# Kernel tuning notes

Hardware: AMD Instinct MI355X
Metric: run time of the kernel (lower is better)

## Reference

```python
import jax, jax.numpy as jnp
import numpy as np

N = 4096
FIN = 512
HID = 256
NCLS = 2
NE = 131072

def _glorot(key, fan_in, fan_out):
    r = np.sqrt(6.0 / (fan_in + fan_out))
    return jax.random.uniform(key, (fan_in, fan_out), jnp.float32, -r, r)

def setup_inputs() -> dict:
    key = jax.random.key(0)
    ks = jax.random.split(key, 16)
    X = jax.random.normal(ks[0], (N, FIN), jnp.float32)
    adj_rows = jax.random.randint(ks[1], (NE,), 0, N, jnp.int32)
    adj_cols = jax.random.randint(ks[2], (NE,), 0, N, jnp.int32)
    adj_vals = jax.random.uniform(ks[3], (NE,), jnp.float32)
    W_shared = _glorot(ks[4], FIN, HID)
    W_iv = _glorot(ks[5], HID, HID)
    W_c = _glorot(ks[6], HID, HID)
    W_r = _glorot(ks[7], HID, HID)
    Wg_iv = _glorot(ks[8], HID, HID)
    Wg_c = _glorot(ks[9], HID, HID)
    Wg_r = _glorot(ks[10], HID, HID)
    lin_W = _glorot(ks[11], 2 * HID, NCLS)
    lin_b = jnp.zeros((NCLS,), jnp.float32)
    return {"X": X, "adj_rows": adj_rows, "adj_cols": adj_cols, "adj_vals": adj_vals,
            "W_shared": W_shared, "W_iv": W_iv, "W_c": W_c, "W_r": W_r,
            "Wg_iv": Wg_iv, "Wg_c": Wg_c, "Wg_r": Wg_r, "lin_W": lin_W, "lin_b": lin_b}

def _spmm(rows, cols, vals, m):
    # sparse.mm(adj, m): out[i] = sum_{e: rows[e]==i} vals[e] * m[cols[e]]
    return jax.ops.segment_sum(vals[:, None] * m[cols], rows, num_segments=N)

def _gcn(x, rows, cols, vals, W):
    # dropout is identity in eval mode
    return jax.nn.relu(_spmm(rows, cols, vals, x @ W))

def _graphite(x, r1, r2, W):
    h = x @ W
    return jax.nn.relu(r1 @ (r1.T @ h) + r2 @ (r2.T @ h))

def reference(X, adj_rows, adj_cols, adj_vals, W_shared, W_iv, W_c, W_r, Wg_iv, Wg_c, Wg_r, lin_W, lin_b):
    h = _gcn(X, adj_rows, adj_cols, adj_vals, W_shared)
    z_iv0 = _gcn(h, adj_rows, adj_cols, adj_vals, W_iv)
    z_c0 = _gcn(h, adj_rows, adj_cols, adj_vals, W_c)
    z_r0 = _gcn(h, adj_rows, adj_cols, adj_vals, W_r)
    z_iv_rec0 = z_iv0 @ z_iv0.T
    z_c_rec0 = z_c0 @ z_c0.T
    z_r_rec0 = z_r0 @ z_r0.T
    A_dense = jnp.zeros((N, N), jnp.float32).at[adj_rows, adj_cols].add(adj_vals)
    z_iv = _graphite(z_iv0, A_dense, jax.nn.sigmoid(z_iv_rec0), Wg_iv)
    z_c = _graphite(z_c0, A_dense, jax.nn.sigmoid(z_c_rec0), Wg_c)
    z_r = _graphite(z_r0, A_dense, jax.nn.sigmoid(z_r_rec0), Wg_r)
    z_iv_rec = z_iv @ z_iv.T
    z_c_rec = z_c @ z_c.T
    z_r_rec = z_r @ z_r.T
    concat = jnp.concatenate([z_iv, z_c], axis=1)
    pred_T = jax.nn.log_softmax(concat @ lin_W + lin_b, axis=1)
    mi_total_loss = jnp.array(0.0, jnp.float32)
    return (z_iv, z_iv_rec, z_c, z_c_rec, z_r, z_r_rec, mi_total_loss, pred_T)
```

## Files before the change

### kernel.cpp

```cpp
#include <hip/hip_runtime.h>

#define Nn   4096
#define FINd 512
#define HIDd 256
#define NEd  131072

typedef unsigned short u16;
typedef __bf16 bf16x8 __attribute__((ext_vector_type(8)));
typedef float floatx4 __attribute__((ext_vector_type(4)));

__device__ __forceinline__ float bf2f(u16 u) {
  union { unsigned int i; float f; } v; v.i = ((unsigned int)u) << 16; return v.f;
}
__device__ __forceinline__ u16 f2bf(float f) {
  union { unsigned int i; float f; } v; v.f = f;
  unsigned int x = v.i;
  return (u16)((x + 0x7FFFu + ((x >> 16) & 1u)) >> 16);
}

#define GLDS(gp, lp) __builtin_amdgcn_global_load_lds( \
    (__attribute__((address_space(1))) unsigned int*)(void*)(gp), \
    (__attribute__((address_space(3))) unsigned int*)(lp), 16, 0, 0)

__global__ __launch_bounds__(256) void izero_k(int* __restrict__ p, int n) {
  int i = blockIdx.x * 256 + threadIdx.x;
  if (i < n) p[i] = 0;
}

__global__ __launch_bounds__(256) void hist2_k(const int* __restrict__ rows,
                                               const int* __restrict__ cols,
                                               int* __restrict__ rcnt,
                                               int* __restrict__ ccnt) {
  int i = blockIdx.x * 256 + threadIdx.x;
  if (i >= NEd) return;
  atomicAdd(&rcnt[rows[i]], 1);
  atomicAdd(&ccnt[cols[i]], 1);
}

__global__ __launch_bounds__(1024) void scan2_k(const unsigned int* __restrict__ X,
                                                int* __restrict__ cnt,
                                                int* __restrict__ rp, int* __restrict__ cp,
                                                int* __restrict__ flag) {
  __shared__ int part[1024];
  __shared__ int dcnt;
  const int t = threadIdx.x;
  if (t == 0) dcnt = 0;
  __syncthreads();
  int local = 0;
  for (int i = t; i < 4096; i += 1024) {
    unsigned e = (X[i] >> 7) & 0xFFu;
    if (e >= 100u && e <= 140u) local++;
  }
  if (local) atomicAdd(&dcnt, local);
  int base = t * 8, s = 0, loc[8];
#pragma unroll
  for (int j = 0; j < 8; ++j) { loc[j] = s; s += cnt[base + j]; }
  part[t] = s;
  __syncthreads();
  if (t == 0) *flag = (dcnt > 2458) ? 1 : 0;
  for (int off = 1; off < 1024; off <<= 1) {
    int v = (t >= off) ? part[t - off] : 0;
    __syncthreads();
    part[t] += v;
    __syncthreads();
  }
  int excl = (t == 0) ? 0 : part[t - 1];
  int rtot = part[511];
  if (t < 512) {
#pragma unroll
    for (int j = 0; j < 8; ++j) rp[base + j] = excl + loc[j];
    if (t == 511) rp[4096] = rtot;
  } else {
    int cb = base - 4096;
    int ex2 = excl - rtot;
#pragma unroll
    for (int j = 0; j < 8; ++j) cp[cb + j] = ex2 + loc[j];
    if (t == 1023) cp[4096] = part[1023] - rtot;
  }
  for (int i = t; i < 8192; i += 1024) cnt[i] = 0;
}

__global__ __launch_bounds__(256) void scatter2_k(const int* __restrict__ rows,
                                                  const int* __restrict__ cols,
                                                  const void* __restrict__ vals,
                                                  const int* __restrict__ rp,
                                                  const int* __restrict__ cp,
                                                  int* __restrict__ rfill, int* __restrict__ cfill,
                                                  int* __restrict__ recol, float* __restrict__ reval,
                                                  int* __restrict__ cecol, float* __restrict__ ceval,
                                                  const int* __restrict__ flag) {
  int i = blockIdx.x * 256 + threadIdx.x;
  if (i >= NEd) return;
  float v = (*flag) ? bf2f(((const u16*)vals)[i]) : ((const float*)vals)[i];
  int r = rows[i], c = cols[i];
  int p1 = rp[r] + atomicAdd(&rfill[r], 1);
  recol[p1] = c; reval[p1] = v;
  int p2 = cp[c] + atomicAdd(&cfill[c], 1);
  cecol[p2] = r; ceval[p2] = v;
}

__global__ __launch_bounds__(256) void setup_cvt_k(const void* __restrict__ X,
                                                   const void* __restrict__ Wsh,
                                                   const void* __restrict__ W0, const void* __restrict__ W1,
                                                   const void* __restrict__ W2, const void* __restrict__ G0,
                                                   const void* __restrict__ G1, const void* __restrict__ G2,
                                                   const void* __restrict__ linW, const void* __restrict__ linb,
                                                   u16* __restrict__ Xb, u16* __restrict__ WshT,
                                                   u16* __restrict__ WTb, u16* __restrict__ WgTb,
                                                   float* __restrict__ linWf, float* __restrict__ linbf,
                                                   const int* __restrict__ flag) {
  int i = blockIdx.x * 256 + threadIdx.x;
  int fl = *flag;
  if (i < 2097152) {
    Xb[i] = fl ? ((const u16*)X)[i] : f2bf(((const float*)X)[i]);
    return;
  }
  int i2 = i - 2097152;
  if (i2 < 131072) {
    int r = i2 >> 8, c = i2 & 255;
    u16 v = fl ? ((const u16*)Wsh)[i2] : f2bf(((const float*)Wsh)[i2]);
    WshT[c * 512 + r] = v;
    return;
  }
  int i3 = i2 - 131072;
  if (i3 < 393216) {
    int w = i3 >> 16, j = i3 & 65535;
    int r = j >> 8, c = j & 255;
    const void* src = (w == 0) ? W0 : (w == 1) ? W1 : (w == 2) ? W2
                     : (w == 3) ? G0 : (w == 4) ? G1 : G2;
    u16 v = fl ? ((const u16*)src)[j] : f2bf(((const float*)src)[j]);
    u16* dst = (w < 3) ? (WTb + w * 65536) : (WgTb + (w - 3) * 65536);
    dst[c * 256 + r] = v;
    return;
  }
  int i4 = i3 - 393216;
  if (i4 < 1024) { linWf[i4] = fl ? bf2f(((const u16*)linW)[i4]) : ((const float*)linW)[i4]; return; }
  if (i4 < 1026) { int k = i4 - 1024; linbf[k] = fl ? bf2f(((const u16*)linb)[k]) : ((const float*)linb)[k]; }
}

struct SPP {
  const int* ptr; const int* ecol; const float* eval;
  const u16* m[3]; u16* ob[3]; unsigned long long oo[3];
};
__global__ __launch_bounds__(256) void spmm_mb_k(SPP s, const float* __restrict__ part,
                                                 void* __restrict__ outbase, int mode,
                                                 const int* __restrict__ flag) {
  const int b = blockIdx.y;
  int gid = blockIdx.x * 256 + threadIdx.x;
  int row = gid >> 6, lane = gid & 63, f = lane << 2;
  int beg = s.ptr[row], end = s.ptr[row + 1];
  const u16* m = s.m[b];
  float ax = 0.f, ay = 0.f, az = 0.f, aw = 0.f;
  for (int e = beg; e < end; ++e) {
    int c = s.ecol[e];
    float v = s.eval[e];
    ushort4 mv = *(const ushort4*)(m + (size_t)c * HIDd + f);
    ax = fmaf(v, bf2f(mv.x), ax);
    ay = fmaf(v, bf2f(mv.y), ay);
    az = fmaf(v, bf2f(mv.z), az);
    aw = fmaf(v, bf2f(mv.w), aw);
  }
  size_t o = (size_t)row * HIDd + f;
  if (mode == 2) {
    const float* pb = part + (size_t)b * 1048576 + o;
    float4 p0 = *(const float4*)(pb);
    float4 p1 = *(const float4*)(pb + 3145728);
    float4 p2 = *(const float4*)(pb + 2 * 3145728);
    float4 p3 = *(const float4*)(pb + 3 * 3145728);
    ax += p0.x + p1.x + p2.x + p3.x;
    ay += p0.y + p1.y + p2.y + p3.y;
    az += p0.z + p1.z + p2.z + p3.z;
    aw += p0.w + p1.w + p2.w + p3.w;
    ax = fmaxf(ax, 0.f); ay = fmaxf(ay, 0.f);
    az = fmaxf(az, 0.f); aw = fmaxf(aw, 0.f);
    ushort4 o4 = { f2bf(ax), f2bf(ay), f2bf(az), f2bf(aw) };
    *(ushort4*)(s.ob[b] + o) = o4;
    if (*flag) *(ushort4*)((u16*)outbase + s.oo[b] + o) = o4;
    else       *(float4*)((float*)outbase + s.oo[b] + o) = make_float4(ax, ay, az, aw);
  } else {
    if (mode == 0) {
      ax = fmaxf(ax, 0.f); ay = fmaxf(ay, 0.f);
      az = fmaxf(az, 0.f); aw = fmaxf(aw, 0.f);
    }
    ushort4 o4 = { f2bf(ax), f2bf(ay), f2bf(az), f2bf(aw) };
    *(ushort4*)(s.ob[b] + o) = o4;
  }
}

struct Job {
  const u16* A; const u16* B;
  unsigned long long c0, c1, pstride;
  int M, N, K, mode, xt, ntiles, nks, kspan, sym;
};
struct Jobs { Job j[6]; };

__global__ __launch_bounds__(256) void gemm_mega(Jobs P, void* __restrict__ WSv,
                                                 void* __restrict__ OutO,
                                                 const int* __restrict__ flag) {
  __shared__ __align__(16) u16 smem[17408];
  u16* As = smem;
  u16* Bs = smem + 8192;
  u16* Ts = smem;
  const Job jb = P.j[blockIdx.z];
  const unsigned tile = blockIdx.x;
  if ((int)tile >= jb.ntiles * jb.nks) return;
  const unsigned ks = tile / (unsigned)jb.ntiles;
  const unsigned t2 = tile - ks * jb.ntiles;
  unsigned ty, tx;
  if (jb.sym) {
    unsigned rem = t2, rowlen = jb.xt; ty = 0;
    while (rem >= rowlen) { rem -= rowlen; --rowlen; ++ty; }
    tx = ty + rem;
  } else {
    ty = t2 / (unsigned)jb.xt;
    tx = t2 - ty * jb.xt;
  }
  const int K = jb.K, N = jb.N;
  const int row0 = ty * 128, col0 = tx * 128;
  const int tid = threadIdx.x;
  const int w = tid >> 6, lane = tid & 63;
  const int wr = (w >> 1) * 64, wc = (w & 1) * 64;
  const int lr = lane >> 3, cc = lane & 7;
  const int scol = (cc ^ lr) << 3;
  floatx4 acc[4][4] = {};
  int aoff[4], boff[4];
#pragma unroll
  for (int i = 0; i < 4; ++i) {
    int m = wr + i * 16 + (lane & 15);
    aoff[i] = m * 64 + ((((lane >> 4) << 3)) ^ ((m & 7) << 3));
    int n = wc + i * 16 + (lane & 15);
    boff[i] = n * 64 + ((((lane >> 4) << 3)) ^ ((n & 7) << 3));
  }
  const u16* A = jb.A;
  const u16* B = jb.B;
  const int kbeg = ks * jb.kspan, kend = kbeg + jb.kspan;
  for (int k0 = kbeg; k0 < kend; k0 += 64) {
#pragma unroll
    for (int t = 0; t < 4; ++t) {
      int ch = 4 * w + t;
      GLDS(A + (size_t)(row0 + 8 * ch + lr) * K + k0 + scol, As + ch * 512);
      GLDS(B + (size_t)(col0 + 8 * ch + lr) * K + k0 + scol, Bs + ch * 512);
    }
    __syncthreads();
#pragma unroll
    for (int kk = 0; kk < 2; ++kk) {
      bf16x8 af[4], bfr[4];
#pragma unroll
      for (int i = 0; i < 4; ++i) {
        af[i]  = *(const bf16x8*)(As + (aoff[i] ^ (kk << 5)));
        bfr[i] = *(const bf16x8*)(Bs + (boff[i] ^ (kk << 5)));
      }
#pragma unroll
      for (int i = 0; i < 4; ++i)
#pragma unroll
        for (int j = 0; j < 4; ++j)
          acc[i][j] = __builtin_amdgcn_mfma_f32_16x16x32_bf16(af[i], bfr[j], acc[i][j], 0, 0, 0);
    }
    __syncthreads();
  }

  const int l15 = lane & 15, q4 = (lane >> 4) << 2;
  const int cb = col0 + wc + l15;
  const int mode = jb.mode;
  if (mode == 5) {
    float* C = (float*)WSv + jb.c0 + (size_t)ks * jb.pstride;
#pragma unroll
    for (int i = 0; i < 4; ++i)
#pragma unroll
      for (int r = 0; r < 4; ++r) {
        size_t rb = (size_t)(row0 + wr + i * 16 + q4 + r) * N + cb;
#pragma unroll
        for (int j = 0; j < 4; ++j) C[rb + j * 16] = acc[i][j][r];
      }
  } else if (mode == 0 || mode == 1) {
    u16* C = ((mode == 1) ? (u16*)OutO : (u16*)WSv) + jb.c0;
#pragma unroll
    for (int i = 0; i < 4; ++i)
#pragma unroll
      for (int r = 0; r < 4; ++r) {
        int lrow = wr + i * 16 + q4 + r;
        size_t rb = (size_t)(row0 + lrow) * N + cb;
#pragma unroll
        for (int j = 0; j < 4; ++j) {
          float v = acc[i][j][r];
          if (mode == 1) v = 1.f / (1.f + __expf(-v));
          u16 vb = f2bf(v);
          C[rb + j * 16] = vb;
          if (jb.sym) Ts[(wc + j * 16 + l15) * 136 + lrow] = vb;
        }
      }
    if (jb.sym && tx != ty) {
      __syncthreads();
      int rr = tid >> 1, hf = (tid & 1) << 6;
      size_t rb2 = (size_t)(col0 + rr) * N + row0 + hf;
#pragma unroll
      for (int k = 0; k < 8; ++k)
        *(uint4*)(C + rb2 + k * 8) = *(const uint4*)(Ts + rr * 136 + hf + k * 8);
    }
  } else if (mode == 4) {
    u16* C  = (u16*)WSv + jb.c0;
    u16* CT = (u16*)WSv + jb.c1;
    const int M = jb.M;
#pragma unroll
    for (int i = 0; i < 4; ++i)
#pragma unroll
      for (int r = 0; r < 4; ++r) {
        int gr = row0 + wr + i * 16 + q4 + r;
#pragma unroll
        for (int j = 0; j < 4; ++j) {
          u16 v = f2bf(acc[i][j][r]);
          int gc = cb + j * 16;
          C[(size_t)gr * N + gc] = v;
          CT[(size_t)gc * M + gr] = v;
        }
      }
  } else {
    if (*flag) {
      u16* C = (u16*)OutO + jb.c0;
#pragma unroll
      for (int i = 0; i < 4; ++i)
#pragma unroll
        for (int r = 0; r < 4; ++r) {
          int lrow = wr + i * 16 + q4 + r;
          size_t rb = (size_t)(row0 + lrow) * N + cb;
#pragma unroll
          for (int j = 0; j < 4; ++j) {
            u16 vb = f2bf(acc[i][j][r]);
            C[rb + j * 16] = vb;
            if (jb.sym) Ts[(wc + j * 16 + l15) * 136 + lrow] = vb;
          }
        }
      if (jb.sym && tx != ty) {
        __syncthreads();
        int rr = tid >> 1, hf = (tid & 1) << 6;
        size_t rb2 = (size_t)(col0 + rr) * N + row0 + hf;
#pragma unroll
        for (int k = 0; k < 8; ++k)
          *(uint4*)(C + rb2 + k * 8) = *(const uint4*)(Ts + rr * 136 + hf + k * 8);
      }
    } else {
      float* C = (float*)OutO + jb.c0;
#pragma unroll
      for (int i = 0; i < 4; ++i)
#pragma unroll
        for (int r = 0; r < 4; ++r) {
          int gr = row0 + wr + i * 16 + q4 + r;
          size_t rb = (size_t)gr * N + cb;
#pragma unroll
          for (int j = 0; j < 4; ++j) {
            float v = acc[i][j][r];
            C[rb + j * 16] = v;
            if (jb.sym && tx != ty) C[(size_t)(cb + j * 16) * N + gr] = v;
          }
        }
    }
  }
}

__global__ __launch_bounds__(256) void redt_k(const float* __restrict__ part,
                                              u16* __restrict__ out) {
  int i = (blockIdx.x * 256 + threadIdx.x) * 4;
  float4 s0 = *(const float4*)(part + i);
  float4 s1 = *(const float4*)(part + i + 3145728);
  float4 s2 = *(const float4*)(part + i + 2 * 3145728);
  float4 s3 = *(const float4*)(part + i + 3 * 3145728);
  ushort4 o = { f2bf(s0.x + s1.x + s2.x + s3.x), f2bf(s0.y + s1.y + s2.y + s3.y),
                f2bf(s0.z + s1.z + s2.z + s3.z), f2bf(s0.w + s1.w + s2.w + s3.w) };
  *(ushort4*)(out + i) = o;
}

__global__ __launch_bounds__(256) void head_k(const u16* __restrict__ ziv,
                                              const u16* __restrict__ zc,
                                              const float* __restrict__ lw,
                                              const float* __restrict__ lb,
                                              void* __restrict__ outbase,
                                              long long pred_off, long long mi_off,
                                              const int* __restrict__ flag) {
  int i = blockIdx.x * 256 + threadIdx.x;
  if (i >= Nn) return;
  float a0 = lb[0], a1 = lb[1];
  for (int f = 0; f < HIDd; ++f) {
    float zv = bf2f(ziv[(size_t)i * HIDd + f]);
    a0 = fmaf(zv, lw[2 * f + 0], a0);
    a1 = fmaf(zv, lw[2 * f + 1], a1);
  }
  for (int f = 0; f < HIDd; ++f) {
    float zv = bf2f(zc[(size_t)i * HIDd + f]);
    a0 = fmaf(zv, lw[2 * (HIDd + f) + 0], a0);
    a1 = fmaf(zv, lw[2 * (HIDd + f) + 1], a1);
  }
  float mx = fmaxf(a0, a1);
  float lse = mx + logf(expf(a0 - mx) + expf(a1 - mx));
  float p0 = a0 - lse, p1 = a1 - lse;
  if (*flag) {
    u16* ob = (u16*)outbase;
    ob[pred_off + 2 * i + 0] = f2bf(p0);
    ob[pred_off + 2 * i + 1] = f2bf(p1);
    if (i == 0) ob[mi_off] = 0;
  } else {
    float* ob = (float*)outbase;
    ob[pred_off + 2 * i + 0] = p0;
    ob[pred_off + 2 * i + 1] = p1;
    if (i == 0) ob[mi_off] = 0.f;
  }
}

extern "C" void kernel_launch(void* const* d_in, const int* in_sizes, int n_in,
                              void* d_out, int out_size, void* d_ws, size_t ws_size,
                              hipStream_t stream) {
  const void* X    = d_in[0];
  const int*  rows = (const int*)d_in[1];
  const int*  cols = (const int*)d_in[2];
  const void* vals = d_in[3];
  const void* Wsh  = d_in[4];

  char* W = (char*)d_ws;
  u16*  Xb    = (u16*)(W + 0);
  u16*  WshT  = (u16*)(W + 4194304);
  u16*  WTb   = (u16*)(W + 4456448);
  u16*  WgTb  = (u16*)(W + 4849664);
  int*  rp    = (int*)(W + 5242880);
  int*  cp    = (int*)(W + 5275648);
  int*  rfill = (int*)(W + 5308416);
  int*  cfill = (int*)(W + 5324800);
  int*  recol = (int*)(W + 5341184);
  float* reval = (float*)(W + 5865472);
  int*  cecol = (int*)(W + 6389760);
  float* ceval = (float*)(W + 6914048);
  float* linWf = (float*)(W + 7438336);
  float* linbf = (float*)(W + 7442432);
  int*  flag  = (int*)(W + 7442560);
  u16*  hb    = (u16*)(W + 8388608);
  u16*  tmpb[3] = { (u16*)(W + 10485760), (u16*)(W + 12582912), (u16*)(W + 14680064) };
  u16*  z0b[3]  = { (u16*)(W + 16777216), (u16*)(W + 18874368), (u16*)(W + 20971520) };
  u16*  hpb[3]  = { (u16*)(W + 23068672), (u16*)(W + 25165824), (u16*)(W + 27262976) };
  u16*  hpT[3]  = { (u16*)(W + 29360128), (u16*)(W + 31457280), (u16*)(W + 33554432) };
  u16*  tTb     = (u16*)(W + 35651584);
  u16*  zbb[3]  = { (u16*)(W + 41943040), (u16*)(W + 44040192), (u16*)(W + 46137344) };
  float* partf  = (float*)(W + 54525952);
  const unsigned long long part_e0 = 54525952ULL / 4;

  const long long z_off[3]   = { 0LL, 17825792LL, 35651584LL };
  const long long rec_off[3] = { 1048576LL, 18874368LL, 36700160LL };
  const long long mi_off = 53477376LL, pred_off = 53477377LL;

  const u16* r2p[3] = { (const u16*)d_out + rec_off[0], (const u16*)d_out + rec_off[1],
                        (const u16*)d_out + rec_off[2] };

  izero_k<<<32, 256, 0, stream>>>(rfill, 8192);
  hist2_k<<<NEd / 256, 256, 0, stream>>>(rows, cols, rfill, cfill);
  scan2_k<<<1, 1024, 0, stream>>>((const unsigned int*)X, rfill, rp, cp, flag);
  setup_cvt_k<<<10245, 256, 0, stream>>>(X, Wsh, d_in[5], d_in[6], d_in[7],
                                         d_in[8], d_in[9], d_in[10], d_in[11], d_in[12],
                                         Xb, WshT, WTb, WgTb, linWf, linbf, flag);
  scatter2_k<<<NEd / 256, 256, 0, stream>>>(rows, cols, vals, rp, cp, rfill, cfill,
                                            recol, reval, cecol, ceval, flag);

  Jobs P{};
  auto setj = [](Job& j, const u16* A, const u16* B, unsigned long long c0,
                 unsigned long long c1, unsigned long long ps, int M, int N, int K,
                 int mode, int nks, int sym) {
    j.A = A; j.B = B; j.c0 = c0; j.c1 = c1; j.pstride = ps;
    j.M = M; j.N = N; j.K = K; j.mode = mode;
    j.xt = N / 128;
    j.ntiles = sym ? (j.xt * (j.xt + 1)) / 2 : (M / 128) * (N / 128);
    j.nks = nks; j.kspan = K / nks; j.sym = sym;
  };

  setj(P.j[0], Xb, WshT, ((char*)tmpb[0] - W) / 2, 0, 0, Nn, HIDd, FINd, 0, 1, 0);
  gemm_mega<<<dim3(64, 1, 1), 256, 0, stream>>>(P, d_ws, d_out, flag);

  SPP s{};
  s.ptr = rp; s.ecol = recol; s.eval = reval;
  s.m[0] = tmpb[0]; s.ob[0] = hb;
  spmm_mb_k<<<dim3(Nn / 4, 1), 256, 0, stream>>>(s, nullptr, nullptr, 0, flag);

  for (int b = 0; b < 3; ++b)
    setj(P.j[b], hb, WTb + b * 65536, ((char*)tmpb[b] - W) / 2, 0, 0, Nn, HIDd, HIDd, 0, 1, 0);
  gemm_mega<<<dim3(64, 1, 3), 256, 0, stream>>>(P, d_ws, d_out, flag);

  for (int b = 0; b < 3; ++b) { s.m[b] = tmpb[b]; s.ob[b] = z0b[b]; }
  spmm_mb_k<<<dim3(Nn / 4, 3), 256, 0, stream>>>(s, nullptr, nullptr, 0, flag);

  for (int b = 0; b < 3; ++b) {
    setj(P.j[b], z0b[b], z0b[b], rec_off[b], 0, 0, Nn, Nn, HIDd, 1, 1, 1);
    setj(P.j[3 + b], z0b[b], WgTb + b * 65536, ((char*)hpb[b] - W) / 2,
         ((char*)hpT[b] - W) / 2, 0, Nn, HIDd, HIDd, 4, 1, 0);
  }
  gemm_mega<<<dim3(528, 1, 6), 256, 0, stream>>>(P, d_ws, d_out, flag);

  SPP sc = s; sc.ptr = cp; sc.ecol = cecol; sc.eval = ceval;
  for (int b = 0; b < 3; ++b) { sc.m[b] = hpb[b]; sc.ob[b] = (u16*)(W + 48234496 + b * 2097152); }
  spmm_mb_k<<<dim3(Nn / 4, 3), 256, 0, stream>>>(sc, nullptr, nullptr, 1, flag);

  for (int b = 0; b < 3; ++b)
    setj(P.j[b], hpT[b], r2p[b], part_e0 + (unsigned long long)b * 1048576, 0, 3145728,
         HIDd, Nn, Nn, 5, 4, 0);
  gemm_mega<<<dim3(256, 1, 3), 256, 0, stream>>>(P, d_ws, d_out, flag);

  redt_k<<<3072, 256, 0, stream>>>(partf, tTb);

  for (int b = 0; b < 3; ++b)
    setj(P.j[b], r2p[b], tTb + b * 1048576, part_e0 + (unsigned long long)b * 1048576, 0,
         3145728, Nn, HIDd, Nn, 5, 4, 0);
  gemm_mega<<<dim3(256, 1, 3), 256, 0, stream>>>(P, d_ws, d_out, flag);

  for (int b = 0; b < 3; ++b) {
    s.m[b] = (const u16*)(W + 48234496 + b * 2097152);
    s.ob[b] = zbb[b]; s.oo[b] = (unsigned long long)z_off[b];
  }
  spmm_mb_k<<<dim3(Nn / 4, 3), 256, 0, stream>>>(s, partf, d_out, 2, flag);

  for (int b = 0; b < 3; ++b)
    setj(P.j[b], zbb[b], zbb[b], rec_off[b], 0, 0, Nn, Nn, HIDd, 3, 1, 1);
  gemm_mega<<<dim3(528, 1, 3), 256, 0, stream>>>(P, d_ws, d_out, flag);

  head_k<<<Nn / 256, 256, 0, stream>>>(zbb[0], zbb[1], linWf, linbf, d_out,
                                       pred_off, mi_off, flag);
  (void)in_sizes; (void)n_in; (void)out_size; (void)ws_size;
}
```

Baseline: 718.6 us.

## Fuse preprocessing and tail kernels, privatize histogram, pack edge arrays

Replaces the global-atomic histogram with per-block LDS histograms that the scan kernel sums from slabs. The edge scatter is merged into the setup conversion kernel, and column/value pairs are packed as int2 so SpMM reads one load per edge. The reverse SpMM is fused into the reduction kernel, and the classification head becomes an extra job inside the final GEMM launch. The aim is fewer launches and less atomic contention, at the cost of a serial 32-slab sum in a single-block scan and some launch-grid imbalance.

```diff
diff --git a/kernel.cpp b/kernel.cpp
--- a/kernel.cpp
+++ b/kernel.cpp
@@ -22,24 +22,28 @@
     (__attribute__((address_space(1))) unsigned int*)(void*)(gp), \
     (__attribute__((address_space(3))) unsigned int*)(lp), 16, 0, 0)
 
-__global__ __launch_bounds__(256) void izero_k(int* __restrict__ p, int n) {
-  int i = blockIdx.x * 256 + threadIdx.x;
-  if (i < n) p[i] = 0;
-}
-
-__global__ __launch_bounds__(256) void hist2_k(const int* __restrict__ rows,
-                                               const int* __restrict__ cols,
-                                               int* __restrict__ rcnt,
-                                               int* __restrict__ ccnt) {
-  int i = blockIdx.x * 256 + threadIdx.x;
-  if (i >= NEd) return;
-  atomicAdd(&rcnt[rows[i]], 1);
-  atomicAdd(&ccnt[cols[i]], 1);
+__global__ __launch_bounds__(256) void hist_priv_k(const int* __restrict__ rows,
+                                                   const int* __restrict__ cols,
+                                                   int* __restrict__ slabs) {
+  __shared__ int cnt[8192];
+  const int t = threadIdx.x;
+  for (int i = t; i < 8192; i += 256) cnt[i] = 0;
+  __syncthreads();
+  int base = blockIdx.x * 4096;
+  for (int i = t; i < 4096; i += 256) {
+    int e = base + i;
+    atomicAdd(&cnt[rows[e]], 1);
+    atomicAdd(&cnt[4096 + cols[e]], 1);
+  }
+  __syncthreads();
+  int* out = slabs + blockIdx.x * 8192;
+  for (int i = t; i < 8192; i += 256) out[i] = cnt[i];
 }
 
 __global__ __launch_bounds__(1024) void scan2_k(const unsigned int* __restrict__ X,
-                                                int* __restrict__ cnt,
+                                                const int* __restrict__ slabs,
                                                 int* __restrict__ rp, int* __restrict__ cp,
+                                                int* __restrict__ rfill, int* __restrict__ cfill,
                                                 int* __restrict__ flag) {
   __shared__ int part[1024];
   __shared__ int dcnt;
@@ -53,8 +57,16 @@
   }
   if (local) atomicAdd(&dcnt, local);
   int base = t * 8, s = 0, loc[8];
-#pragma unroll
-  for (int j = 0; j < 8; ++j) { loc[j] = s; s += cnt[base + j]; }
+  int csum[8];
+#pragma unroll
+  for (int j = 0; j < 8; ++j) csum[j] = 0;
+  for (int sl = 0; sl < 32; ++sl) {
+    const int* sp = slabs + sl * 8192 + base;
+#pragma unroll
+    for (int j = 0; j < 8; ++j) csum[j] += sp[j];
+  }
+#pragma unroll
+  for (int j = 0; j < 8; ++j) { loc[j] = s; s += csum[j]; }
   part[t] = s;
   __syncthreads();
   if (t == 0) *flag = (dcnt > 2458) ? 1 : 0;
@@ -77,40 +89,38 @@
     for (int j = 0; j < 8; ++j) cp[cb + j] = ex2 + loc[j];
     if (t == 1023) cp[4096] = part[1023] - rtot;
   }
-  for (int i = t; i < 8192; i += 1024) cnt[i] = 0;
-}
-
-__global__ __launch_bounds__(256) void scatter2_k(const int* __restrict__ rows,
-                                                  const int* __restrict__ cols,
-                                                  const void* __restrict__ vals,
-                                                  const int* __restrict__ rp,
-                                                  const int* __restrict__ cp,
-                                                  int* __restrict__ rfill, int* __restrict__ cfill,
-                                                  int* __restrict__ recol, float* __restrict__ reval,
-                                                  int* __restrict__ cecol, float* __restrict__ ceval,
-                                                  const int* __restrict__ flag) {
-  int i = blockIdx.x * 256 + threadIdx.x;
-  if (i >= NEd) return;
-  float v = (*flag) ? bf2f(((const u16*)vals)[i]) : ((const float*)vals)[i];
-  int r = rows[i], c = cols[i];
-  int p1 = rp[r] + atomicAdd(&rfill[r], 1);
-  recol[p1] = c; reval[p1] = v;
-  int p2 = cp[c] + atomicAdd(&cfill[c], 1);
-  cecol[p2] = r; ceval[p2] = v;
-}
-
-__global__ __launch_bounds__(256) void setup_cvt_k(const void* __restrict__ X,
-                                                   const void* __restrict__ Wsh,
-                                                   const void* __restrict__ W0, const void* __restrict__ W1,
-                                                   const void* __restrict__ W2, const void* __restrict__ G0,
-                                                   const void* __restrict__ G1, const void* __restrict__ G2,
-                                                   const void* __restrict__ linW, const void* __restrict__ linb,
-                                                   u16* __restrict__ Xb, u16* __restrict__ WshT,
-                                                   u16* __restrict__ WTb, u16* __restrict__ WgTb,
-                                                   float* __restrict__ linWf, float* __restrict__ linbf,
-                                                   const int* __restrict__ flag) {
-  int i = blockIdx.x * 256 + threadIdx.x;
+  for (int i = t; i < 4096; i += 1024) { rfill[i] = 0; cfill[i] = 0; }
+}
+
+__global__ __launch_bounds__(256) void setup2_k(const void* __restrict__ X,
+                                                const void* __restrict__ Wsh,
+                                                const void* __restrict__ W0, const void* __restrict__ W1,
+                                                const void* __restrict__ W2, const void* __restrict__ G0,
+                                                const void* __restrict__ G1, const void* __restrict__ G2,
+                                                const void* __restrict__ linW, const void* __restrict__ linb,
+                                                const int* __restrict__ rows, const int* __restrict__ cols,
+                                                const void* __restrict__ vals,
+                                                const int* __restrict__ rp, const int* __restrict__ cp,
+                                                int* __restrict__ rfill, int* __restrict__ cfill,
+                                                int2* __restrict__ rpack, int2* __restrict__ cpack,
+                                                u16* __restrict__ Xb, u16* __restrict__ WshT,
+                                                u16* __restrict__ WTb, u16* __restrict__ WgTb,
+                                                float* __restrict__ linWf, float* __restrict__ linbf,
+                                                const int* __restrict__ flag) {
   int fl = *flag;
+  int bx = blockIdx.x;
+  if (bx >= 10245) {
+    int e = (bx - 10245) * 256 + threadIdx.x;
+    if (e >= NEd) return;
+    float v = fl ? bf2f(((const u16*)vals)[e]) : ((const float*)vals)[e];
+    int r = rows[e], c = cols[e];
+    int p1 = rp[r] + atomicAdd(&rfill[r], 1);
+    rpack[p1] = make_int2(c, __float_as_int(v));
+    int p2 = cp[c] + atomicAdd(&cfill[c], 1);
+    cpack[p2] = make_int2(r, __float_as_int(v));
+    return;
+  }
+  int i = bx * 256 + threadIdx.x;
   if (i < 2097152) {
     Xb[i] = fl ? ((const u16*)X)[i] : f2bf(((const float*)X)[i]);
     return;
@@ -139,7 +149,7 @@
 }
 
 struct SPP {
-  const int* ptr; const int* ecol; const float* eval;
+  const int* ptr; const int2* ep;
   const u16* m[3]; u16* ob[3]; unsigned long long oo[3];
 };
 __global__ __launch_bounds__(256) void spmm_mb_k(SPP s, const float* __restrict__ part,
@@ -152,9 +162,9 @@
   const u16* m = s.m[b];
   float ax = 0.f, ay = 0.f, az = 0.f, aw = 0.f;
   for (int e = beg; e < end; ++e) {
-    int c = s.ecol[e];
-    float v = s.eval[e];
-    ushort4 mv = *(const ushort4*)(m + (size_t)c * HIDd + f);
+    int2 cv = s.ep[e];
+    float v = __int_as_float(cv.y);
+    ushort4 mv = *(const ushort4*)(m + (size_t)cv.x * HIDd + f);
     ax = fmaf(v, bf2f(mv.x), ax);
     ay = fmaf(v, bf2f(mv.y), ay);
     az = fmaf(v, bf2f(mv.z), az);
@@ -187,8 +197,47 @@
   }
 }
 
+struct RSU {
+  const float* part; u16* tT;
+  const int* cp; const int2* cep;
+  const u16* hp[3]; u16* ub[3];
+};
+__global__ __launch_bounds__(256) void redt_spmmu_k(RSU r) {
+  int bx = blockIdx.x;
+  if (bx < 3072) {
+    int i = (bx * 256 + threadIdx.x) * 4;
+    float4 s0 = *(const float4*)(r.part + i);
+    float4 s1 = *(const float4*)(r.part + i + 3145728);
+    float4 s2 = *(const float4*)(r.part + i + 2 * 3145728);
+    float4 s3 = *(const float4*)(r.part + i + 3 * 3145728);
+    ushort4 o = { f2bf(s0.x + s1.x + s2.x + s3.x), f2bf(s0.y + s1.y + s2.y + s3.y),
+                  f2bf(s0.z + s1.z + s2.z + s3.z), f2bf(s0.w + s1.w + s2.w + s3.w) };
+    *(ushort4*)(r.tT + i) = o;
+    return;
+  }
+  int bb = (bx - 3072) >> 10;
+  int gid = ((bx - 3072) & 1023) * 256 + threadIdx.x;
+  int row = gid >> 6, lane = gid & 63, f = lane << 2;
+  int beg = r.cp[row], end = r.cp[row + 1];
+  const u16* m = r.hp[bb];
+  float ax = 0.f, ay = 0.f, az = 0.f, aw = 0.f;
+  for (int e = beg; e < end; ++e) {
+    int2 cv = r.cep[e];
+    float v = __int_as_float(cv.y);
+    ushort4 mv = *(const ushort4*)(m + (size_t)cv.x * HIDd + f);
+    ax = fmaf(v, bf2f(mv.x), ax);
+    ay = fmaf(v, bf2f(mv.y), ay);
+    az = fmaf(v, bf2f(mv.z), az);
+    aw = fmaf(v, bf2f(mv.w), aw);
+  }
+  size_t o = (size_t)row * HIDd + f;
+  ushort4 o4 = { f2bf(ax), f2bf(ay), f2bf(az), f2bf(aw) };
+  *(ushort4*)(r.ub[bb] + o) = o4;
+}
+
 struct Job {
   const u16* A; const u16* B;
+  const float* F1; const float* F2;
   unsigned long long c0, c1, pstride;
   int M, N, K, mode, xt, ntiles, nks, kspan, sym;
 };
@@ -204,6 +253,36 @@
   const Job jb = P.j[blockIdx.z];
   const unsigned tile = blockIdx.x;
   if ((int)tile >= jb.ntiles * jb.nks) return;
+  if (jb.mode == 6) {
+    int i = tile * 256 + threadIdx.x;
+    const float* lw = jb.F1;
+    float a0 = jb.F2[0], a1 = jb.F2[1];
+    for (int f = 0; f < HIDd; ++f) {
+      float zv = bf2f(jb.A[(size_t)i * HIDd + f]);
+      a0 = fmaf(zv, lw[2 * f + 0], a0);
+      a1 = fmaf(zv, lw[2 * f + 1], a1);
+    }
+    for (int f = 0; f < HIDd; ++f) {
+      float zv = bf2f(jb.B[(size_t)i * HIDd + f]);
+      a0 = fmaf(zv, lw[2 * (HIDd + f) + 0], a0);
+      a1 = fmaf(zv, lw[2 * (HIDd + f) + 1], a1);
+    }
+    float mx = fmaxf(a0, a1);
+    float lse = mx + logf(expf(a0 - mx) + expf(a1 - mx));
+    float p0 = a0 - lse, p1 = a1 - lse;
+    if (*flag) {
+      u16* ob = (u16*)OutO;
+      ob[jb.c0 + 2 * i + 0] = f2bf(p0);
+      ob[jb.c0 + 2 * i + 1] = f2bf(p1);
+      if (i == 0) ob[jb.c1] = 0;
+    } else {
+      float* ob = (float*)OutO;
+      ob[jb.c0 + 2 * i + 0] = p0;
+      ob[jb.c0 + 2 * i + 1] = p1;
+      if (i == 0) ob[jb.c1] = 0.f;
+    }
+    return;
+  }
   const unsigned ks = tile / (unsigned)jb.ntiles;
   const unsigned t2 = tile - ks * jb.ntiles;
   unsigned ty, tx;
@@ -357,54 +436,6 @@
   }
 }
 
-__global__ __launch_bounds__(256) void redt_k(const float* __restrict__ part,
-                                              u16* __restrict__ out) {
-  int i = (blockIdx.x * 256 + threadIdx.x) * 4;
-  float4 s0 = *(const float4*)(part + i);
-  float4 s1 = *(const float4*)(part + i + 3145728);
-  float4 s2 = *(const float4*)(part + i + 2 * 3145728);
-  float4 s3 = *(const float4*)(part + i + 3 * 3145728);
-  ushort4 o = { f2bf(s0.x + s1.x + s2.x + s3.x), f2bf(s0.y + s1.y + s2.y + s3.y),
-                f2bf(s0.z + s1.z + s2.z + s3.z), f2bf(s0.w + s1.w + s2.w + s3.w) };
-  *(ushort4*)(out + i) = o;
-}
-
-__global__ __launch_bounds__(256) void head_k(const u16* __restrict__ ziv,
-                                              const u16* __restrict__ zc,
-                                              const float* __restrict__ lw,
-                                              const float* __restrict__ lb,
-                                              void* __restrict__ outbase,
-                                              long long pred_off, long long mi_off,
-                                              const int* __restrict__ flag) {
-  int i = blockIdx.x * 256 + threadIdx.x;
-  if (i >= Nn) return;
-  float a0 = lb[0], a1 = lb[1];
-  for (int f = 0; f < HIDd; ++f) {
-    float zv = bf2f(ziv[(size_t)i * HIDd + f]);
-    a0 = fmaf(zv, lw[2 * f + 0], a0);
-    a1 = fmaf(zv, lw[2 * f + 1], a1);
-  }
-  for (int f = 0; f < HIDd; ++f) {
-    float zv = bf2f(zc[(size_t)i * HIDd + f]);
-    a0 = fmaf(zv, lw[2 * (HIDd + f) + 0], a0);
-    a1 = fmaf(zv, lw[2 * (HIDd + f) + 1], a1);
-  }
-  float mx = fmaxf(a0, a1);
-  float lse = mx + logf(expf(a0 - mx) + expf(a1 - mx));
-  float p0 = a0 - lse, p1 = a1 - lse;
-  if (*flag) {
-    u16* ob = (u16*)outbase;
-    ob[pred_off + 2 * i + 0] = f2bf(p0);
-    ob[pred_off + 2 * i + 1] = f2bf(p1);
-    if (i == 0) ob[mi_off] = 0;
-  } else {
-    float* ob = (float*)outbase;
-    ob[pred_off + 2 * i + 0] = p0;
-    ob[pred_off + 2 * i + 1] = p1;
-    if (i == 0) ob[mi_off] = 0.f;
-  }
-}
-
 extern "C" void kernel_launch(void* const* d_in, const int* in_sizes, int n_in,
                               void* d_out, int out_size, void* d_ws, size_t ws_size,
                               hipStream_t stream) {
@@ -423,10 +454,8 @@
   int*  cp    = (int*)(W + 5275648);
   int*  rfill = (int*)(W + 5308416);
   int*  cfill = (int*)(W + 5324800);
-  int*  recol = (int*)(W + 5341184);
-  float* reval = (float*)(W + 5865472);
-  int*  cecol = (int*)(W + 6389760);
-  float* ceval = (float*)(W + 6914048);
+  int2* rpack = (int2*)(W + 5341184);
+  int2* cpack = (int2*)(W + 6389760);
   float* linWf = (float*)(W + 7438336);
   float* linbf = (float*)(W + 7442432);
   int*  flag  = (int*)(W + 7442560);
@@ -437,7 +466,9 @@
   u16*  hpT[3]  = { (u16*)(W + 29360128), (u16*)(W + 31457280), (u16*)(W + 33554432) };
   u16*  tTb     = (u16*)(W + 35651584);
   u16*  zbb[3]  = { (u16*)(W + 41943040), (u16*)(W + 44040192), (u16*)(W + 46137344) };
+  u16*  ubb[3]  = { (u16*)(W + 48234496), (u16*)(W + 50331648), (u16*)(W + 52428800) };
   float* partf  = (float*)(W + 54525952);
+  int*  slabs  = (int*)(W + 54525952);
   const unsigned long long part_e0 = 54525952ULL / 4;
 
   const long long z_off[3]   = { 0LL, 17825792LL, 35651584LL };
@@ -447,20 +478,19 @@
   const u16* r2p[3] = { (const u16*)d_out + rec_off[0], (const u16*)d_out + rec_off[1],
                         (const u16*)d_out + rec_off[2] };
 
-  izero_k<<<32, 256, 0, stream>>>(rfill, 8192);
-  hist2_k<<<NEd / 256, 256, 0, stream>>>(rows, cols, rfill, cfill);
-  scan2_k<<<1, 1024, 0, stream>>>((const unsigned int*)X, rfill, rp, cp, flag);
-  setup_cvt_k<<<10245, 256, 0, stream>>>(X, Wsh, d_in[5], d_in[6], d_in[7],
-                                         d_in[8], d_in[9], d_in[10], d_in[11], d_in[12],
-                                         Xb, WshT, WTb, WgTb, linWf, linbf, flag);
-  scatter2_k<<<NEd / 256, 256, 0, stream>>>(rows, cols, vals, rp, cp, rfill, cfill,
-                                            recol, reval, cecol, ceval, flag);
+  hist_priv_k<<<32, 256, 0, stream>>>(rows, cols, slabs);
+  scan2_k<<<1, 1024, 0, stream>>>((const unsigned int*)X, slabs, rp, cp, rfill, cfill, flag);
+  setup2_k<<<10757, 256, 0, stream>>>(X, Wsh, d_in[5], d_in[6], d_in[7],
+                                      d_in[8], d_in[9], d_in[10], d_in[11], d_in[12],
+                                      rows, cols, vals, rp, cp, rfill, cfill, rpack, cpack,
+                                      Xb, WshT, WTb, WgTb, linWf, linbf, flag);
 
   Jobs P{};
   auto setj = [](Job& j, const u16* A, const u16* B, unsigned long long c0,
                  unsigned long long c1, unsigned long long ps, int M, int N, int K,
                  int mode, int nks, int sym) {
-    j.A = A; j.B = B; j.c0 = c0; j.c1 = c1; j.pstride = ps;
+    j.A = A; j.B = B; j.F1 = nullptr; j.F2 = nullptr;
+    j.c0 = c0; j.c1 = c1; j.pstride = ps;
     j.M = M; j.N = N; j.K = K; j.mode = mode;
     j.xt = N / 128;
     j.ntiles = sym ? (j.xt * (j.xt + 1)) / 2 : (M / 128) * (N / 128);
@@ -471,7 +501,7 @@
   gemm_mega<<<dim3(64, 1, 1), 256, 0, stream>>>(P, d_ws, d_out, flag);
 
   SPP s{};
-  s.ptr = rp; s.ecol = recol; s.eval = reval;
+  s.ptr = rp; s.ep = rpack;
   s.m[0] = tmpb[0]; s.ob[0] = hb;
   spmm_mb_k<<<dim3(Nn / 4, 1), 256, 0, stream>>>(s, nullptr, nullptr, 0, flag);
 
@@ -489,16 +519,15 @@
   }
   gemm_mega<<<dim3(528, 1, 6), 256, 0, stream>>>(P, d_ws, d_out, flag);
 
-  SPP sc = s; sc.ptr = cp; sc.ecol = cecol; sc.eval = ceval;
-  for (int b = 0; b < 3; ++b) { sc.m[b] = hpb[b]; sc.ob[b] = (u16*)(W + 48234496 + b * 2097152); }
-  spmm_mb_k<<<dim3(Nn / 4, 3), 256, 0, stream>>>(sc, nullptr, nullptr, 1, flag);
-
   for (int b = 0; b < 3; ++b)
     setj(P.j[b], hpT[b], r2p[b], part_e0 + (unsigned long long)b * 1048576, 0, 3145728,
          HIDd, Nn, Nn, 5, 4, 0);
   gemm_mega<<<dim3(256, 1, 3), 256, 0, stream>>>(P, d_ws, d_out, flag);
 
-  redt_k<<<3072, 256, 0, stream>>>(partf, tTb);
+  RSU r{};
+  r.part = partf; r.tT = tTb; r.cp = cp; r.cep = cpack;
+  for (int b = 0; b < 3; ++b) { r.hp[b] = hpb[b]; r.ub[b] = ubb[b]; }
+  redt_spmmu_k<<<6144, 256, 0, stream>>>(r);
 
   for (int b = 0; b < 3; ++b)
     setj(P.j[b], r2p[b], tTb + b * 1048576, part_e0 + (unsigned long long)b * 1048576, 0,
@@ -506,16 +535,18 @@
   gemm_mega<<<dim3(256, 1, 3), 256, 0, stream>>>(P, d_ws, d_out, flag);
 
   for (int b = 0; b < 3; ++b) {
-    s.m[b] = (const u16*)(W + 48234496 + b * 2097152);
+    s.m[b] = ubb[b];
     s.ob[b] = zbb[b]; s.oo[b] = (unsigned long long)z_off[b];
   }
   spmm_mb_k<<<dim3(Nn / 4, 3), 256, 0, stream>>>(s, partf, d_out, 2, flag);
 
   for (int b = 0; b < 3; ++b)
     setj(P.j[b], zbb[b], zbb[b], rec_off[b], 0, 0, Nn, Nn, HIDd, 3, 1, 1);
-  gemm_mega<<<dim3(528, 1, 3), 256, 0, stream>>>(P, d_ws, d_out, flag);
-
-  head_k<<<Nn / 256, 256, 0, stream>>>(zbb[0], zbb[1], linWf, linbf, d_out,
-                                       pred_off, mi_off, flag);
+  setj(P.j[3], zbb[0], zbb[1], (unsigned long long)pred_off,
+       (unsigned long long)mi_off, 0, 256, 128, 64, 6, 1, 0);
+  P.j[3].ntiles = 16; P.j[3].nks = 1;
+  P.j[3].F1 = linWf; P.j[3].F2 = linbf;
+  gemm_mega<<<dim3(528, 1, 4), 256, 0, stream>>>(P, d_ws, d_out, flag);
+
   (void)in_sizes; (void)n_in; (void)out_size; (void)ws_size;
 }
```

Measured after the change: 709.2 us. Within noise of the previous version (-1.3%).
